# Optimization experiments

Measured on AMD Instinct MI355X. Metric: run time of the kernel, lower is better.

Reference implementation:

```python
import jax, jax.numpy as jnp
import numpy as np

EPSILON = 1e-06

def setup_inputs() -> dict:
    key = jax.random.key(0)
    k1, k2, k3 = jax.random.split(key, 3)
    B, M, W, H = 64, 16384, 128, 8
    memory = jax.random.normal(k1, (B, M, W), dtype=jnp.float32)
    keys = jax.random.normal(k2, (B, H, W), dtype=jnp.float32)
    strengths = jax.random.normal(k3, (B, H), dtype=jnp.float32)
    return {"memory": memory, "keys": keys, "strengths": strengths}

def reference(memory, keys, strengths):
    # scores: [B, H, M] dot product of each key with each memory slot
    scores = jnp.einsum('bhw,bmw->bhm', keys, memory)
    memory_norms = jnp.linalg.norm(memory, axis=-1)          # [B, M]
    keys_norms = jnp.linalg.norm(keys, axis=-1)              # [B, H]
    denom = memory_norms[:, None, :] * keys_norms[:, :, None] + EPSILON  # [B, H, M]
    normed_scores = scores / denom
    # weighted softmax with softplus strength
    adjusted = jax.nn.softplus(strengths)[..., None]          # [B, H, 1]
    weighted = normed_scores * adjusted
    return jax.nn.softmax(weighted, axis=-1)                  # [B, H, M]
```

## Files before the change

### kernel.cpp

```cpp
#include <hip/hip_runtime.h>
#include <cmath>

namespace {

constexpr int kB = 64;
constexpr int kM = 16384;
constexpr int kW = 128;
constexpr int kH = 8;
constexpr float kEps = 1e-6f;

__global__ __launch_bounds__(256) void cw_stats(
    const float* __restrict__ keys,
    const float* __restrict__ strengths,
    float* __restrict__ ws)
{
  const int b = blockIdx.x;
  const int t = threadIdx.x;
  const int h = t >> 5, p = t & 31;
  const float4 v = ((const float4*)(keys + ((size_t)b * kH + h) * kW))[p];
  float a = v.x * v.x + v.y * v.y + v.z * v.z + v.w * v.w;
  #pragma unroll
  for (int off = 16; off > 0; off >>= 1) a += __shfl_xor(a, off);
  if (p == 0) {
    ws[b * kH + h] = sqrtf(a);
    const float x = strengths[b * kH + h];
    ws[kB * kH + b * kH + h] = fmaxf(x, 0.f) + log1pf(__expf(-fabsf(x)));
  }
}

__global__ __launch_bounds__(256) void cw_scores(
    const float* __restrict__ mem,
    const float* __restrict__ keys,
    const float* __restrict__ ws,
    float* __restrict__ out)
{
  __shared__ float4 s_mem[64 * 32];
  __shared__ float4 s_keys[kH * 32];
  __shared__ float s_red[4 * 64 * 9];
  __shared__ float s_kn[kH], s_adj[kH];

  const int t = threadIdx.x;
  const int b = blockIdx.x >> 8;
  const int m0 = (blockIdx.x & 255) << 6;

  s_keys[t] = ((const float4*)(keys + (size_t)b * kH * kW))[t];
  if (t < kH) {
    s_kn[t] = ws[b * kH + t];
    s_adj[t] = ws[kB * kH + b * kH + t];
  }

  const float4* g = (const float4*)(mem + ((size_t)b * kM + m0) * kW);
  #pragma unroll
  for (int r = 0; r < 8; ++r) {
    const int gi = r * 256 + t;
    const int s = gi >> 5, c = gi & 31;
    s_mem[s * 32 + (c ^ (s & 7))] = g[gi];
  }
  __syncthreads();

  const int q = t >> 6, lane = t & 63;
  float d[kH];
  float n = 0.f;
  #pragma unroll
  for (int h = 0; h < kH; ++h) d[h] = 0.f;

  #pragma unroll
  for (int j = 0; j < 8; ++j) {
    const int c = q * 8 + j;
    const float4 v = s_mem[lane * 32 + (c ^ (lane & 7))];
    n = fmaf(v.x, v.x, fmaf(v.y, v.y, fmaf(v.z, v.z, fmaf(v.w, v.w, n))));
    #pragma unroll
    for (int h = 0; h < kH; ++h) {
      const float4 kk = s_keys[h * 32 + c];
      d[h] = fmaf(v.x, kk.x, fmaf(v.y, kk.y, fmaf(v.z, kk.z, fmaf(v.w, kk.w, d[h]))));
    }
  }

  float* rp = s_red + (q * 64 + lane) * 9;
  #pragma unroll
  for (int h = 0; h < kH; ++h) rp[h] = d[h];
  rp[8] = n;
  __syncthreads();

  if (t < 64) {
    float f[9];
    #pragma unroll
    for (int k = 0; k < 9; ++k)
      f[k] = s_red[t * 9 + k] + s_red[(64 + t) * 9 + k] +
             s_red[(128 + t) * 9 + k] + s_red[(192 + t) * 9 + k];
    const float mn = sqrtf(f[8]);
    float* op = out + (size_t)b * kH * kM + m0 + t;
    #pragma unroll
    for (int h = 0; h < kH; ++h)
      op[h * kM] = s_adj[h] * f[h] / fmaf(mn, s_kn[h], kEps);
  }
}

__global__ __launch_bounds__(256) void cw_softmax(float* __restrict__ out)
{
  __shared__ float red[16];

  const int tid = threadIdx.x;
  const int wave = tid >> 6, lane = tid & 63;
  float4* p4 = (float4*)(out + (size_t)blockIdx.x * kM);

  float4 vs[16];
  float lmax = -INFINITY;
  #pragma unroll
  for (int k = 0; k < 16; ++k) {
    vs[k] = p4[k * 256 + tid];
    lmax = fmaxf(lmax, fmaxf(fmaxf(vs[k].x, vs[k].y), fmaxf(vs[k].z, vs[k].w)));
  }
  #pragma unroll
  for (int off = 32; off > 0; off >>= 1) lmax = fmaxf(lmax, __shfl_xor(lmax, off));
  if (lane == 0) red[wave] = lmax;
  __syncthreads();
  const float bmax = fmaxf(fmaxf(red[0], red[1]), fmaxf(red[2], red[3]));

  float lsum = 0.f;
  #pragma unroll
  for (int k = 0; k < 16; ++k) {
    vs[k].x = __expf(vs[k].x - bmax);
    vs[k].y = __expf(vs[k].y - bmax);
    vs[k].z = __expf(vs[k].z - bmax);
    vs[k].w = __expf(vs[k].w - bmax);
    lsum += (vs[k].x + vs[k].y) + (vs[k].z + vs[k].w);
  }
  #pragma unroll
  for (int off = 32; off > 0; off >>= 1) lsum += __shfl_xor(lsum, off);
  if (lane == 0) red[8 + wave] = lsum;
  __syncthreads();
  const float inv = 1.f / ((red[8] + red[9]) + (red[10] + red[11]));

  #pragma unroll
  for (int k = 0; k < 16; ++k) {
    vs[k].x *= inv; vs[k].y *= inv; vs[k].z *= inv; vs[k].w *= inv;
    p4[k * 256 + tid] = vs[k];
  }
}

}

extern "C" void kernel_launch(void* const* d_in, const int* in_sizes, int n_in,
                              void* d_out, int out_size, void* d_ws, size_t ws_size,
                              hipStream_t stream) {
  (void)in_sizes; (void)n_in; (void)ws_size; (void)out_size;
  const float* mem       = (const float*)d_in[0];
  const float* keys      = (const float*)d_in[1];
  const float* strengths = (const float*)d_in[2];
  float* out = (float*)d_out;
  float* wsf = (float*)d_ws;

  cw_stats<<<dim3(kB), dim3(256), 0, stream>>>(keys, strengths, wsf);
  cw_scores<<<dim3(kB * (kM / 64)), dim3(256), 0, stream>>>(mem, keys, wsf, out);
  cw_softmax<<<dim3(kB * kH), dim3(256), 0, stream>>>(out);
}
```

Baseline: 699.9 us.

## Compute one memory row per thread directly from global, dropping LDS staging

The scores kernel now assigns each thread one full memory row of 128 floats and loads it straight from global memory, instead of staging 64 rows in LDS and reducing partial dot products across four waves. Keys and norms are read as uniform global/scalar loads, and split accumulators add a little ILP. This removes LDS traffic, two barriers and the cross-wave reduction. The cost is that the loads are now strided: adjacent lanes read addresses 512 bytes apart, so global coalescing becomes poor and the kernel depends on cache lines being reused across the per-thread loads.

Measured after the change: 725.9 us. 1.04x slower.

```diff
diff --git a/kernel.cpp b/kernel.cpp
--- a/kernel.cpp
+++ b/kernel.cpp
@@ -28,71 +28,65 @@
   }
 }
 
-__global__ __launch_bounds__(256) void cw_scores(
+__global__ __launch_bounds__(256, 4) void cw_scores(
     const float* __restrict__ mem,
     const float* __restrict__ keys,
     const float* __restrict__ ws,
     float* __restrict__ out)
 {
-  __shared__ float4 s_mem[64 * 32];
-  __shared__ float4 s_keys[kH * 32];
-  __shared__ float s_red[4 * 64 * 9];
-  __shared__ float s_kn[kH], s_adj[kH];
+  const int t = threadIdx.x;
+  const int b = blockIdx.x >> 6;
+  const int m = ((blockIdx.x & 63) << 8) + t;
 
-  const int t = threadIdx.x;
-  const int b = blockIdx.x >> 8;
-  const int m0 = (blockIdx.x & 255) << 6;
+  const float4* __restrict__ gm =
+      (const float4*)(mem + ((size_t)b * kM + m) * kW);
+  const float* __restrict__ kb = keys + (size_t)b * kH * kW;
 
-  s_keys[t] = ((const float4*)(keys + (size_t)b * kH * kW))[t];
-  if (t < kH) {
-    s_kn[t] = ws[b * kH + t];
-    s_adj[t] = ws[kB * kH + b * kH + t];
-  }
-
-  const float4* g = (const float4*)(mem + ((size_t)b * kM + m0) * kW);
+  float d0[kH], d1[kH];
+  float n0 = 0.f, n1 = 0.f;
   #pragma unroll
-  for (int r = 0; r < 8; ++r) {
-    const int gi = r * 256 + t;
-    const int s = gi >> 5, c = gi & 31;
-    s_mem[s * 32 + (c ^ (s & 7))] = g[gi];
-  }
-  __syncthreads();
-
-  const int q = t >> 6, lane = t & 63;
-  float d[kH];
-  float n = 0.f;
-  #pragma unroll
-  for (int h = 0; h < kH; ++h) d[h] = 0.f;
+  for (int h = 0; h < kH; ++h) { d0[h] = 0.f; d1[h] = 0.f; }
 
   #pragma unroll
-  for (int j = 0; j < 8; ++j) {
-    const int c = q * 8 + j;
-    const float4 v = s_mem[lane * 32 + (c ^ (lane & 7))];
-    n = fmaf(v.x, v.x, fmaf(v.y, v.y, fmaf(v.z, v.z, fmaf(v.w, v.w, n))));
+  for (int cg = 0; cg < 8; ++cg) {
+    float4 v[4];
     #pragma unroll
-    for (int h = 0; h < kH; ++h) {
-      const float4 kk = s_keys[h * 32 + c];
-      d[h] = fmaf(v.x, kk.x, fmaf(v.y, kk.y, fmaf(v.z, kk.z, fmaf(v.w, kk.w, d[h]))));
+    for (int j = 0; j < 4; ++j) v[j] = gm[cg * 4 + j];
+
+    #pragma unroll
+    for (int j = 0; j < 4; ++j) {
+      const int c4 = (cg * 4 + j) * 4;
+      if (cg & 1) {
+        n1 = fmaf(v[j].x, v[j].x, fmaf(v[j].y, v[j].y,
+             fmaf(v[j].z, v[j].z, fmaf(v[j].w, v[j].w, n1))));
+      } else {
+        n0 = fmaf(v[j].x, v[j].x, fmaf(v[j].y, v[j].y,
+             fmaf(v[j].z, v[j].z, fmaf(v[j].w, v[j].w, n0))));
+      }
+      #pragma unroll
+      for (int h = 0; h < kH; ++h) {
+        const float k0 = kb[h * kW + c4 + 0];
+        const float k1 = kb[h * kW + c4 + 1];
+        const float k2 = kb[h * kW + c4 + 2];
+        const float k3 = kb[h * kW + c4 + 3];
+        if (cg & 1) {
+          d1[h] = fmaf(v[j].x, k0, fmaf(v[j].y, k1,
+                  fmaf(v[j].z, k2, fmaf(v[j].w, k3, d1[h]))));
+        } else {
+          d0[h] = fmaf(v[j].x, k0, fmaf(v[j].y, k1,
+                  fmaf(v[j].z, k2, fmaf(v[j].w, k3, d0[h]))));
+        }
+      }
     }
   }
 
-  float* rp = s_red + (q * 64 + lane) * 9;
+  const float nrm = sqrtf(n0 + n1);
+  float* op = out + (size_t)b * kH * kM + m;
   #pragma unroll
-  for (int h = 0; h < kH; ++h) rp[h] = d[h];
-  rp[8] = n;
-  __syncthreads();
-
-  if (t < 64) {
-    float f[9];
-    #pragma unroll
-    for (int k = 0; k < 9; ++k)
-      f[k] = s_red[t * 9 + k] + s_red[(64 + t) * 9 + k] +
-             s_red[(128 + t) * 9 + k] + s_red[(192 + t) * 9 + k];
-    const float mn = sqrtf(f[8]);
-    float* op = out + (size_t)b * kH * kM + m0 + t;
-    #pragma unroll
-    for (int h = 0; h < kH; ++h)
-      op[h * kM] = s_adj[h] * f[h] / fmaf(mn, s_kn[h], kEps);
+  for (int h = 0; h < kH; ++h) {
+    const float kn  = ws[b * kH + h];
+    const float adj = ws[kB * kH + b * kH + h];
+    op[(size_t)h * kM] = adj * (d0[h] + d1[h]) / fmaf(nrm, kn, kEps);
   }
 }
 
@@ -152,6 +146,6 @@
   float* wsf = (float*)d_ws;
 
   cw_stats<<<dim3(kB), dim3(256), 0, stream>>>(keys, strengths, wsf);
-  cw_scores<<<dim3(kB * (kM / 64)), dim3(256), 0, stream>>>(mem, keys, wsf, out);
+  cw_scores<<<dim3(kB * (kM / 256)), dim3(256), 0, stream>>>(mem, keys, wsf, out);
   cw_softmax<<<dim3(kB * kH), dim3(256), 0, stream>>>(out);
 }
```
